# Kernel tuning notes

Measured on AMD Instinct MI355X. Metric: run time of the kernel, lower is better.

Reference implementation:

```python
import jax, jax.numpy as jnp
import numpy as np

B, N, D, H, C = 2048, 6, 2048, 1024, 200  # batch, nodes/graph, feat dim, hidden, classes
ALPHA = 0.015   # distance decay in edge weight
SCALE = 24.0    # weight rescale after mean-subtraction + clamp


def setup_inputs() -> dict:
    key = jax.random.key(0)
    k1, k2, k3, k4 = jax.random.split(key, 4)
    part_feats = jax.random.normal(k1, (B, N, D), dtype=jnp.float32)
    # cdds columns: [score, y0, x0, y1, x1, idx]; only cols 1:5 (box coords) are used
    cdds = jax.random.uniform(k2, (B, N, 6), dtype=jnp.float32) * 448.0
    fc_w = jax.random.normal(k3, (2 * D, H), dtype=jnp.float32) * 0.02
    fc_b = jnp.zeros((H,), dtype=jnp.float32)
    cls_w = jax.random.normal(k4, (H, C), dtype=jnp.float32) * 0.02
    cls_b = jnp.zeros((C,), dtype=jnp.float32)
    return {"part_feats": part_feats, "cdds": cdds, "fc_w": fc_w, "fc_b": fc_b,
            "cls_w": cls_w, "cls_b": cls_b}


def reference(part_feats, cdds, fc_w, fc_b, cls_w, cls_b):
    # --- edge weights on per-sample complete graph (apply_edges) ---
    loc = cdds[:, :, 1:5]                      # (B, N, 4) = (y0, x0, y1, x1)
    cy = (loc[..., 0] + loc[..., 2]) * 0.5     # node center y, (B, N)
    cx = (loc[..., 1] + loc[..., 3]) * 0.5     # node center x, (B, N)
    dx = cx[:, :, None] - cx[:, None, :]       # (B, N, N) pairwise
    dy = cy[:, :, None] - cy[:, None, :]
    d2 = dx * dx + dy * dy
    mask = ~jnp.eye(N, dtype=bool)             # off-diagonal = real edges (30 per graph)
    dist = jnp.sqrt(jnp.where(mask, d2, 1.0))  # safe sqrt off the diagonal
    w0 = jnp.where(mask, jnp.exp(-ALPHA * dist), 0.0)
    mean_w = jnp.sum(w0, axis=(1, 2), keepdims=True) / (N * (N - 1))  # mean over 30 edges
    w = SCALE * jnp.maximum(w0 - mean_w, 0.0) * mask                  # (B, N, N), w[b,u,v]
    # --- update_all: u_mul_e + mean over the (N-1) incoming edges per node ---
    hidden = jnp.einsum('buv,bud->bvd', w, part_feats) / (N - 1)      # (B, N, D)
    # --- node MLP + graph mean readout + classifier ---
    node_ft = jnp.concatenate([hidden, part_feats], axis=-1) @ fc_w + fc_b  # (B, N, H)
    g_ft = node_ft.mean(axis=1)                                             # (B, H)
    return g_ft @ cls_w + cls_b                                             # (B, C)
```

## Files before the change

### kernel.cpp

```cpp
#include <hip/hip_runtime.h>
#include <math.h>

namespace {
constexpr int NB = 2048;
constexpr int NNODE = 6;
constexpr int DD = 2048;
constexpr int HH = 1024;
constexpr int CC = 200;
constexpr int K2 = 2 * DD;
constexpr int NPAD = 256;
constexpr int ZS2 = 16;
constexpr float ALPHA_C = 0.015f;
constexpr float SCALE_C = 24.0f;

constexpr int G1_BLOCKS = (K2 / 64) * (NPAD / 64);
constexpr int BV_BLOCKS = 25;
constexpr int PQ_BASE = G1_BLOCKS + BV_BLOCKS;
}

typedef __attribute__((ext_vector_type(8))) short bf16x8;
typedef __attribute__((ext_vector_type(4))) float f32x4;

static __device__ __forceinline__ unsigned short f2bf(float x) {
    union { float f; unsigned int u; } v; v.f = x;
    unsigned int r = v.u + 0x7FFFu + ((v.u >> 16) & 1u);
    return (unsigned short)(r >> 16);
}

static __device__ __forceinline__ unsigned pack2(float a, float b) {
    return (unsigned)f2bf(a) | ((unsigned)f2bf(b) << 16);
}

static __device__ __forceinline__ void compute_s_wave(const float* __restrict__ cdds,
                                                      int b, float sv[NNODE]) {
    const int lane = threadIdx.x & 63;
    const int u = lane >> 3;
    const int v = lane & 7;
    const float* cd = cdds + (size_t)b * 36;
    float w = 0.f;
    const bool valid = (u < 6) & (v < 6) & (u != v);
    if (u < 6 && v < 6 && u != v) {
        float cyu = (cd[u * 6 + 1] + cd[u * 6 + 3]) * 0.5f;
        float cxu = (cd[u * 6 + 2] + cd[u * 6 + 4]) * 0.5f;
        float cyv = (cd[v * 6 + 1] + cd[v * 6 + 3]) * 0.5f;
        float cxv = (cd[v * 6 + 2] + cd[v * 6 + 4]) * 0.5f;
        float dx = cxu - cxv, dy = cyu - cyv;
        w = expf(-ALPHA_C * sqrtf(dx * dx + dy * dy));
    }
    float s = w;
#pragma unroll
    for (int m = 32; m >= 1; m >>= 1) s += __shfl_xor(s, m);
    float mean = s * (1.f / 30.f);
    float tt = valid ? fmaxf(w - mean, 0.f) : 0.f;
    tt += __shfl_xor(tt, 1);
    tt += __shfl_xor(tt, 2);
    tt += __shfl_xor(tt, 4);
    float su = SCALE_C * tt * 0.2f;
#pragma unroll
    for (int uu = 0; uu < NNODE; ++uu) sv[uu] = __shfl(su, uu * 8);
}

__global__ __launch_bounds__(256) void k_front(const float* __restrict__ pf,
                                               const float* __restrict__ cdds,
                                               const float* __restrict__ fc_w,
                                               const float* __restrict__ cls_w,
                                               const float* __restrict__ fc_b,
                                               const float* __restrict__ cls_b,
                                               unsigned short* __restrict__ pq,
                                               unsigned short* __restrict__ Mt,
                                               float* __restrict__ bvec)
{
    __shared__ short As[64][68];
    __shared__ short Bs[64][68];
    __shared__ float red[256];
    const int bx = blockIdx.x;
    const int t = threadIdx.x;

    if (bx >= PQ_BASE) {
        const int b = bx - PQ_BASE;
        float sv[NNODE];
        compute_s_wave(cdds, b, sv);
        const int d = t << 3;
        const float* base = pf + (size_t)b * NNODE * DD + d;
        float4 p0 = {0, 0, 0, 0}, p1 = {0, 0, 0, 0};
        float4 q0 = {0, 0, 0, 0}, q1 = {0, 0, 0, 0};
#pragma unroll
        for (int u = 0; u < NNODE; ++u) {
            float4 a0 = *(const float4*)(base + (size_t)u * DD);
            float4 a1 = *(const float4*)(base + (size_t)u * DD + 4);
            float s = sv[u];
            p0.x = fmaf(s, a0.x, p0.x); p0.y = fmaf(s, a0.y, p0.y);
            p0.z = fmaf(s, a0.z, p0.z); p0.w = fmaf(s, a0.w, p0.w);
            p1.x = fmaf(s, a1.x, p1.x); p1.y = fmaf(s, a1.y, p1.y);
            p1.z = fmaf(s, a1.z, p1.z); p1.w = fmaf(s, a1.w, p1.w);
            q0.x += a0.x; q0.y += a0.y; q0.z += a0.z; q0.w += a0.w;
            q1.x += a1.x; q1.y += a1.y; q1.z += a1.z; q1.w += a1.w;
        }
        unsigned short* o = pq + (size_t)b * K2;
        uint4 po, qo;
        po.x = pack2(p0.x, p0.y); po.y = pack2(p0.z, p0.w);
        po.z = pack2(p1.x, p1.y); po.w = pack2(p1.z, p1.w);
        qo.x = pack2(q0.x, q0.y); qo.y = pack2(q0.z, q0.w);
        qo.z = pack2(q1.x, q1.y); qo.w = pack2(q1.z, q1.w);
        *(uint4*)(o + d) = po;
        *(uint4*)(o + DD + d) = qo;
        return;
    }

    if (bx >= G1_BLOCKS) {
        const int bb = bx - G1_BLOCKS;
        int c8 = t & 7;
        int hs = t >> 3;
        int c = bb * 8 + c8;
        float acc = 0.f;
        for (int h = hs; h < HH; h += 32)
            acc += fc_b[h] * cls_w[(size_t)h * CC + c];
        red[t] = acc;
        __syncthreads();
        for (int s = 128; s >= 8; s >>= 1) {
            if (t < s) red[t] += red[t + s];
            __syncthreads();
        }
        if (t < 8) bvec[c] = red[t] + cls_b[c];
        return;
    }

    const int lane = t & 63;
    const int wid = t >> 6;
    const int wm = wid >> 1, wn = wid & 1;
    const int bm = (bx >> 2) * 64;
    const int bn = (bx & 3) * 64;

    f32x4 acc[2][2] = {};

    for (int k0 = 0; k0 < HH; k0 += 64) {
#pragma unroll
        for (int c = 0; c < 4; ++c) {
            int i = t + c * 256;
            int row = i >> 4;
            int k4 = (i & 15) << 2;
            float4 v = *(const float4*)(fc_w + (size_t)(bm + row) * HH + k0 + k4);
            ushort4 o;
            o.x = f2bf(v.x); o.y = f2bf(v.y); o.z = f2bf(v.z); o.w = f2bf(v.w);
            *(ushort4*)&As[row][k4] = o;
        }
#pragma unroll
        for (int c = 0; c < 4; ++c) {
            int i = t + c * 256;
            int kr = i >> 4;
            int n4 = (i & 15) << 2;
            const float* sp = cls_w + (size_t)(k0 + kr) * CC + bn + n4;
            float4 v = {0.f, 0.f, 0.f, 0.f};
            if (bn + n4 + 3 < CC) {
                v = *(const float4*)sp;
            } else {
                if (bn + n4 + 0 < CC) v.x = sp[0];
                if (bn + n4 + 1 < CC) v.y = sp[1];
                if (bn + n4 + 2 < CC) v.z = sp[2];
                if (bn + n4 + 3 < CC) v.w = sp[3];
            }
            Bs[n4 + 0][kr] = (short)f2bf(v.x);
            Bs[n4 + 1][kr] = (short)f2bf(v.y);
            Bs[n4 + 2][kr] = (short)f2bf(v.z);
            Bs[n4 + 3][kr] = (short)f2bf(v.w);
        }
        __syncthreads();
#pragma unroll
        for (int ks = 0; ks < 2; ++ks) {
            int kk = ks * 32 + ((lane >> 4) << 3);
            int ar = lane & 15;
            bf16x8 a0 = *(const bf16x8*)&As[wm * 32 + ar][kk];
            bf16x8 a1 = *(const bf16x8*)&As[wm * 32 + 16 + ar][kk];
            bf16x8 b0 = *(const bf16x8*)&Bs[wn * 32 + ar][kk];
            bf16x8 b1 = *(const bf16x8*)&Bs[wn * 32 + 16 + ar][kk];
            acc[0][0] = __builtin_amdgcn_mfma_f32_16x16x32_bf16(a0, b0, acc[0][0], 0, 0, 0);
            acc[0][1] = __builtin_amdgcn_mfma_f32_16x16x32_bf16(a0, b1, acc[0][1], 0, 0, 0);
            acc[1][0] = __builtin_amdgcn_mfma_f32_16x16x32_bf16(a1, b0, acc[1][0], 0, 0, 0);
            acc[1][1] = __builtin_amdgcn_mfma_f32_16x16x32_bf16(a1, b1, acc[1][1], 0, 0, 0);
        }
        __syncthreads();
    }
#pragma unroll
    for (int fm = 0; fm < 2; ++fm)
#pragma unroll
        for (int fn = 0; fn < 2; ++fn) {
            int gm0 = bm + wm * 32 + fm * 16 + ((lane >> 4) << 2);
            int gn = bn + wn * 32 + fn * 16 + (lane & 15);
            ushort4 o;
            o.x = f2bf(acc[fm][fn][0]); o.y = f2bf(acc[fm][fn][1]);
            o.z = f2bf(acc[fm][fn][2]); o.w = f2bf(acc[fm][fn][3]);
            *(ushort4*)(Mt + (size_t)gn * K2 + gm0) = o;
        }
}

__global__ __launch_bounds__(256) void k_gemm2(const unsigned short* __restrict__ A,
                                               const unsigned short* __restrict__ Bt,
                                               float* __restrict__ part)
{
    __shared__ short As[64][72];
    __shared__ short Bs[256][72];
    const int t = threadIdx.x;
    const int lane = t & 63;
    const int wid = t >> 6;
    const int wr = wid >> 1, wc = wid & 1;
    const int bm = blockIdx.x * 64;
    const int z = blockIdx.y;
    const int kbase = z * (K2 / ZS2);

    f32x4 acc[2][8] = {};

    for (int k0 = kbase; k0 < kbase + K2 / ZS2; k0 += 64) {
#pragma unroll
        for (int c = 0; c < 2; ++c) {
            int i = t + c * 256;
            int row = i >> 3;
            int k8 = (i & 7) << 3;
            *(uint4*)&As[row][k8] =
                *(const uint4*)(A + (size_t)(bm + row) * K2 + k0 + k8);
        }
#pragma unroll
        for (int c = 0; c < 8; ++c) {
            int i = t + c * 256;
            int n = i >> 3;
            int k8 = (i & 7) << 3;
            *(uint4*)&Bs[n][k8] =
                *(const uint4*)(Bt + (size_t)n * K2 + k0 + k8);
        }
        __syncthreads();
#pragma unroll
        for (int ks = 0; ks < 2; ++ks) {
            int kk = ks * 32 + ((lane >> 4) << 3);
            int ar = lane & 15;
            bf16x8 a0 = *(const bf16x8*)&As[wr * 32 + ar][kk];
            bf16x8 a1 = *(const bf16x8*)&As[wr * 32 + 16 + ar][kk];
#pragma unroll
            for (int fn = 0; fn < 8; ++fn) {
                bf16x8 b = *(const bf16x8*)&Bs[wc * 128 + fn * 16 + ar][kk];
                acc[0][fn] = __builtin_amdgcn_mfma_f32_16x16x32_bf16(a0, b, acc[0][fn], 0, 0, 0);
                acc[1][fn] = __builtin_amdgcn_mfma_f32_16x16x32_bf16(a1, b, acc[1][fn], 0, 0, 0);
            }
        }
        __syncthreads();
    }
#pragma unroll
    for (int fm = 0; fm < 2; ++fm)
#pragma unroll
        for (int fn = 0; fn < 8; ++fn) {
            int gm0 = bm + wr * 32 + fm * 16 + ((lane >> 4) << 2);
            int gn = wc * 128 + fn * 16 + (lane & 15);
#pragma unroll
            for (int r = 0; r < 4; ++r)
                part[((size_t)z * NB + gm0 + r) * NPAD + gn] = acc[fm][fn][r];
        }
}

__global__ __launch_bounds__(256) void k_combine(const float* __restrict__ part,
                                                 const float* __restrict__ bvec,
                                                 float* __restrict__ out)
{
    int idx = blockIdx.x * blockDim.x + threadIdx.x;
    if (idx >= NB * CC) return;
    int b = idx / CC;
    int c = idx - b * CC;
    float s = 0.f;
#pragma unroll
    for (int z = 0; z < ZS2; ++z)
        s += part[((size_t)z * NB + b) * NPAD + c];
    out[idx] = s * (1.f / 6.f) + bvec[c];
}

extern "C" void kernel_launch(void* const* d_in, const int* in_sizes, int n_in,
                              void* d_out, int out_size, void* d_ws, size_t ws_size,
                              hipStream_t stream)
{
    const float* part_feats = (const float*)d_in[0];
    const float* cdds = (const float*)d_in[1];
    const float* fc_w = (const float*)d_in[2];
    const float* fc_b = (const float*)d_in[3];
    const float* cls_w = (const float*)d_in[4];
    const float* cls_b = (const float*)d_in[5];
    float* out = (float*)d_out;

    char* ws = (char*)d_ws;
    size_t off = 0;
    unsigned short* pq = (unsigned short*)(ws + off); off += (size_t)NB * K2 * 2;
    unsigned short* Mt = (unsigned short*)(ws + off); off += (size_t)NPAD * K2 * 2;
    float* part = (float*)(ws + off);                 off += (size_t)ZS2 * NB * NPAD * 4;
    float* bvec = (float*)(ws + off);                 off += 256 * 4;

    k_front<<<dim3(PQ_BASE + NB), dim3(256), 0, stream>>>(
        part_feats, cdds, fc_w, cls_w, fc_b, cls_b, pq, Mt, bvec);
    k_gemm2<<<dim3(NB / 64, ZS2), dim3(256), 0, stream>>>(pq, Mt, part);
    k_combine<<<dim3((NB * CC + 255) / 256), dim3(256), 0, stream>>>(part, bvec, out);
}
```

Baseline: 76.79 us.

## Split pq reduction into its own kernel with more blocks and early loads

Moves the per-sample weighted node reduction out of the fused front kernel into a separate k_pq launch. Each sample now spans two blocks of four floats per thread, and all six node loads are issued before the edge-weight computation so memory latency overlaps with the shuffle math. The aim is better memory-level parallelism and simpler per-kernel register use for the bandwidth-bound reduction. The cost is an extra kernel launch and the loss of concurrency between the weight-prep GEMM blocks and the pq blocks, which previously shared one grid.

New measurement: 88.01 us. +14.6%, slower.

```diff
diff --git a/kernel.cpp b/kernel.cpp
--- a/kernel.cpp
+++ b/kernel.cpp
@@ -15,7 +15,6 @@
 
 constexpr int G1_BLOCKS = (K2 / 64) * (NPAD / 64);
 constexpr int BV_BLOCKS = 25;
-constexpr int PQ_BASE = G1_BLOCKS + BV_BLOCKS;
 }
 
 typedef __attribute__((ext_vector_type(8))) short bf16x8;
@@ -60,52 +59,18 @@
     for (int uu = 0; uu < NNODE; ++uu) sv[uu] = __shfl(su, uu * 8);
 }
 
-__global__ __launch_bounds__(256) void k_front(const float* __restrict__ pf,
-                                               const float* __restrict__ cdds,
-                                               const float* __restrict__ fc_w,
-                                               const float* __restrict__ cls_w,
-                                               const float* __restrict__ fc_b,
-                                               const float* __restrict__ cls_b,
-                                               unsigned short* __restrict__ pq,
-                                               unsigned short* __restrict__ Mt,
-                                               float* __restrict__ bvec)
+__global__ __launch_bounds__(256) void k_prep(const float* __restrict__ fc_w,
+                                              const float* __restrict__ cls_w,
+                                              const float* __restrict__ fc_b,
+                                              const float* __restrict__ cls_b,
+                                              unsigned short* __restrict__ Mt,
+                                              float* __restrict__ bvec)
 {
     __shared__ short As[64][68];
     __shared__ short Bs[64][68];
     __shared__ float red[256];
     const int bx = blockIdx.x;
     const int t = threadIdx.x;
-
-    if (bx >= PQ_BASE) {
-        const int b = bx - PQ_BASE;
-        float sv[NNODE];
-        compute_s_wave(cdds, b, sv);
-        const int d = t << 3;
-        const float* base = pf + (size_t)b * NNODE * DD + d;
-        float4 p0 = {0, 0, 0, 0}, p1 = {0, 0, 0, 0};
-        float4 q0 = {0, 0, 0, 0}, q1 = {0, 0, 0, 0};
-#pragma unroll
-        for (int u = 0; u < NNODE; ++u) {
-            float4 a0 = *(const float4*)(base + (size_t)u * DD);
-            float4 a1 = *(const float4*)(base + (size_t)u * DD + 4);
-            float s = sv[u];
-            p0.x = fmaf(s, a0.x, p0.x); p0.y = fmaf(s, a0.y, p0.y);
-            p0.z = fmaf(s, a0.z, p0.z); p0.w = fmaf(s, a0.w, p0.w);
-            p1.x = fmaf(s, a1.x, p1.x); p1.y = fmaf(s, a1.y, p1.y);
-            p1.z = fmaf(s, a1.z, p1.z); p1.w = fmaf(s, a1.w, p1.w);
-            q0.x += a0.x; q0.y += a0.y; q0.z += a0.z; q0.w += a0.w;
-            q1.x += a1.x; q1.y += a1.y; q1.z += a1.z; q1.w += a1.w;
-        }
-        unsigned short* o = pq + (size_t)b * K2;
-        uint4 po, qo;
-        po.x = pack2(p0.x, p0.y); po.y = pack2(p0.z, p0.w);
-        po.z = pack2(p1.x, p1.y); po.w = pack2(p1.z, p1.w);
-        qo.x = pack2(q0.x, q0.y); qo.y = pack2(q0.z, q0.w);
-        qo.z = pack2(q1.x, q1.y); qo.w = pack2(q1.z, q1.w);
-        *(uint4*)(o + d) = po;
-        *(uint4*)(o + DD + d) = qo;
-        return;
-    }
 
     if (bx >= G1_BLOCKS) {
         const int bb = bx - G1_BLOCKS;
@@ -193,6 +158,53 @@
         }
 }
 
+__global__ __launch_bounds__(256) void k_pq(const float* __restrict__ pf,
+                                            const float* __restrict__ cdds,
+                                            unsigned short* __restrict__ pq)
+{
+    const int bid = blockIdx.x;
+    const int b = bid >> 1;
+    const int d = ((bid & 1) << 10) + (threadIdx.x << 2);
+
+    const float* base = pf + (size_t)b * NNODE * DD + d;
+    float4 v0 = *(const float4*)(base + 0 * DD);
+    float4 v1 = *(const float4*)(base + 1 * DD);
+    float4 v2 = *(const float4*)(base + 2 * DD);
+    float4 v3 = *(const float4*)(base + 3 * DD);
+    float4 v4 = *(const float4*)(base + 4 * DD);
+    float4 v5 = *(const float4*)(base + 5 * DD);
+
+    float sv[NNODE];
+    compute_s_wave(cdds, b, sv);
+
+    float4 q;
+    q.x = v0.x + v1.x + v2.x + v3.x + v4.x + v5.x;
+    q.y = v0.y + v1.y + v2.y + v3.y + v4.y + v5.y;
+    q.z = v0.z + v1.z + v2.z + v3.z + v4.z + v5.z;
+    q.w = v0.w + v1.w + v2.w + v3.w + v4.w + v5.w;
+
+    float4 p = {0.f, 0.f, 0.f, 0.f};
+    p.x = fmaf(sv[0], v0.x, p.x); p.y = fmaf(sv[0], v0.y, p.y);
+    p.z = fmaf(sv[0], v0.z, p.z); p.w = fmaf(sv[0], v0.w, p.w);
+    p.x = fmaf(sv[1], v1.x, p.x); p.y = fmaf(sv[1], v1.y, p.y);
+    p.z = fmaf(sv[1], v1.z, p.z); p.w = fmaf(sv[1], v1.w, p.w);
+    p.x = fmaf(sv[2], v2.x, p.x); p.y = fmaf(sv[2], v2.y, p.y);
+    p.z = fmaf(sv[2], v2.z, p.z); p.w = fmaf(sv[2], v2.w, p.w);
+    p.x = fmaf(sv[3], v3.x, p.x); p.y = fmaf(sv[3], v3.y, p.y);
+    p.z = fmaf(sv[3], v3.z, p.z); p.w = fmaf(sv[3], v3.w, p.w);
+    p.x = fmaf(sv[4], v4.x, p.x); p.y = fmaf(sv[4], v4.y, p.y);
+    p.z = fmaf(sv[4], v4.z, p.z); p.w = fmaf(sv[4], v4.w, p.w);
+    p.x = fmaf(sv[5], v5.x, p.x); p.y = fmaf(sv[5], v5.y, p.y);
+    p.z = fmaf(sv[5], v5.z, p.z); p.w = fmaf(sv[5], v5.w, p.w);
+
+    unsigned short* o = pq + (size_t)b * K2;
+    ushort4 pb, qb;
+    pb.x = f2bf(p.x); pb.y = f2bf(p.y); pb.z = f2bf(p.z); pb.w = f2bf(p.w);
+    qb.x = f2bf(q.x); qb.y = f2bf(q.y); qb.z = f2bf(q.z); qb.w = f2bf(q.w);
+    *(ushort4*)(o + d) = pb;
+    *(ushort4*)(o + DD + d) = qb;
+}
+
 __global__ __launch_bounds__(256) void k_gemm2(const unsigned short* __restrict__ A,
                                                const unsigned short* __restrict__ Bt,
                                                float* __restrict__ part)
@@ -288,8 +300,9 @@
     float* part = (float*)(ws + off);                 off += (size_t)ZS2 * NB * NPAD * 4;
     float* bvec = (float*)(ws + off);                 off += 256 * 4;
 
-    k_front<<<dim3(PQ_BASE + NB), dim3(256), 0, stream>>>(
-        part_feats, cdds, fc_w, cls_w, fc_b, cls_b, pq, Mt, bvec);
+    k_prep<<<dim3(G1_BLOCKS + BV_BLOCKS), dim3(256), 0, stream>>>(
+        fc_w, cls_w, fc_b, cls_b, Mt, bvec);
+    k_pq<<<dim3(NB * 2), dim3(256), 0, stream>>>(part_feats, cdds, pq);
     k_gemm2<<<dim3(NB / 64, ZS2), dim3(256), 0, stream>>>(pq, Mt, part);
     k_combine<<<dim3((NB * CC + 255) / 256), dim3(256), 0, stream>>>(part, bvec, out);
 }
```
